# Kernel tuning notes

Hardware: AMD Instinct MI355X
Metric: run time of the kernel (lower is better)

## Reference

```python
import jax, jax.numpy as jnp
import numpy as np

CHUNK = 4096
DECAY = 0.99
EPS = 1e-5


def setup_inputs() -> dict:
    key = jax.random.key(0)
    k1, k2, k3, k4 = jax.random.split(key, 4)
    z = jax.random.normal(k1, (32, 64, 32, 32), dtype=jnp.float32)
    codebook = jax.random.normal(k2, (8192, 64), dtype=jnp.float32)
    cluster_size = jax.random.uniform(k3, (8192,), dtype=jnp.float32)
    embed_avg = jax.random.normal(k4, (8192, 64), dtype=jnp.float32)
    return {"z": z, "codebook": codebook, "cluster_size": cluster_size, "embed_avg": embed_avg}


def _nearest_indices(vectors, codebook):
    """Chunked fp32 squared-L2 nearest-neighbor search (matches _nearest_indices)."""
    cb = codebook.astype(jnp.float32)
    c2 = jnp.sum(cb * cb, axis=1)  # [K]

    def chunk_fn(chunk):
        v = chunk.astype(jnp.float32)  # [CHUNK, D]
        d = jnp.sum(v * v, axis=1, keepdims=True) + c2[None, :] - 2.0 * (v @ cb.T)
        return jnp.argmin(d, axis=1)

    n, d = vectors.shape  # n divisible by CHUNK by construction
    chunks = vectors.reshape(n // CHUNK, CHUNK, d)
    return jax.lax.map(chunk_fn, chunks).reshape(-1)


def reference(z, codebook, cluster_size, embed_avg):
    B, C, H, W = z.shape
    K = codebook.shape[0]
    # [B,C,H,W] -> [N,C]
    vectors = jnp.transpose(z, (0, 2, 3, 1)).reshape(-1, C)
    N = vectors.shape[0]

    indices = _nearest_indices(vectors, codebook)  # [N] int
    quantized = jnp.transpose(codebook[indices].reshape(B, H, W, C), (0, 3, 1, 2))

    # commitment loss (codebook learned via EMA, so only encoder side differentiable)
    vq_loss = jnp.mean((jax.lax.stop_gradient(quantized) - z) ** 2)
    # straight-through estimator
    quantized_st = z + jax.lax.stop_gradient(quantized - z)

    # code usage statistics
    counts = jax.ops.segment_sum(jnp.ones((N,), jnp.float32), indices, num_segments=K)
    avg_probs = counts / N
    perplexity = jnp.exp(-jnp.sum(avg_probs * jnp.log(avg_probs + 1e-10)))
    active_codes = jnp.sum(counts > 0).astype(jnp.int32)

    # EMA update (scatter-add accumulation + Laplace-smoothed normalization)
    sums = jax.ops.segment_sum(vectors.astype(jnp.float32), indices, num_segments=K)
    new_cluster_size = DECAY * cluster_size + (1.0 - DECAY) * counts
    new_embed_avg = DECAY * embed_avg + (1.0 - DECAY) * sums
    n_total = jnp.sum(new_cluster_size)
    smoothed = (new_cluster_size + EPS) / (n_total + K * EPS) * n_total
    new_codebook = new_embed_avg / smoothed[:, None]

    return (quantized_st, indices, vq_loss, perplexity, active_codes,
            new_codebook, new_cluster_size, new_embed_avg)
```

## Files before the change

kernel.cpp:

```cpp
#include <hip/hip_runtime.h>
#include <math.h>

typedef unsigned short u16;
typedef unsigned int u32;
typedef __attribute__((ext_vector_type(8))) short short8;
typedef __attribute__((ext_vector_type(4))) float f32x4;

#define NVEC   32768
#define DIMV   64
#define KC     8192
#define NKCH   4
#define CHK    2048
#define HW     1024
#define BPLANE 65536

#define OFF_Q    0
#define OFF_IDX  2097152
#define OFF_LOSS 2129920
#define OFF_PPL  2129921
#define OFF_ACT  2129922
#define OFF_NCB  2129923
#define OFF_NCS  2654211
#define OFF_NEA  2662403

#define WS_COUNTS 0
#define WS_SCAL   8192
#define WS_C2     8200
#define WS_CANDD  16392
#define WS_CANDI  147464
#define WS_CBH    278536
#define WS_CBM    540680
#define WS_CBL    802824

__device__ __forceinline__ u16 f2bf(float x) {
    u32 u = __float_as_uint(x);
    u += 0x7fffu + ((u >> 16) & 1u);
    return (u16)(u >> 16);
}
__device__ __forceinline__ float bf2f(u16 h) {
    return __uint_as_float(((u32)h) << 16);
}

__global__ __launch_bounds__(256) void cbsplit_kernel(const float* __restrict__ cb,
                                                      u16* __restrict__ cbh,
                                                      u16* __restrict__ cbm,
                                                      u16* __restrict__ cbl,
                                                      float* __restrict__ c2) {
    const int t = threadIdx.x;
    const int k = blockIdx.x * 4 + (t >> 6);
    const int d = t & 63;
    const int idx = k * DIMV + d;
    float x = cb[idx];
    u16 hb = f2bf(x);  float fh = bf2f(hb);
    float r1 = x - fh; u16 mb = f2bf(r1); float fm = bf2f(mb);
    float r2 = r1 - fm; u16 lb = f2bf(r2);
    cbh[idx] = hb; cbm[idx] = mb; cbl[idx] = lb;
    float s = x * x;
    for (int off = 32; off > 0; off >>= 1) s += __shfl_down(s, off, 64);
    if (d == 0) c2[k] = s;
}

__global__ __launch_bounds__(256, 2) void nn_kernel(const float* __restrict__ z,
                                                    const u16* __restrict__ cbh,
                                                    const u16* __restrict__ cbm,
                                                    const u16* __restrict__ cbl,
                                                    const float* __restrict__ c2,
                                                    float* __restrict__ candD,
                                                    int* __restrict__ candI) {
    const int l  = threadIdx.x & 63;
    const int w  = threadIdx.x >> 6;
    const int vg = blockIdx.x;
    const int kc = blockIdx.y;
    const int m0 = vg * 256 + w * 64;
    const int lr = l & 15;
    const int lg = l >> 4;

    short8 A[4][3][2];
#pragma unroll
    for (int i = 0; i < 4; ++i) {
        const int vec = m0 + i * 16 + lr;
        const float* zp = z + (size_t)(vec >> 10) * BPLANE + (vec & 1023);
#pragma unroll
        for (int s = 0; s < 2; ++s) {
            short8 ah, am, al;
#pragma unroll
            for (int e = 0; e < 8; ++e) {
                const int k = s * 32 + lg * 8 + e;
                float x = zp[k * HW];
                u16 hb = f2bf(x);   float fh = bf2f(hb);
                float r1 = x - fh;  u16 mb = f2bf(r1); float fm = bf2f(mb);
                float r2 = r1 - fm; u16 lb = f2bf(r2);
                ah[e] = (short)hb; am[e] = (short)mb; al[e] = (short)lb;
            }
            A[i][0][s] = ah; A[i][1][s] = am; A[i][2][s] = al;
        }
    }

    float bestv[4][4];
    int   bestn[4][4];
#pragma unroll
    for (int i = 0; i < 4; ++i)
#pragma unroll
        for (int r = 0; r < 4; ++r) { bestv[i][r] = -3.4e38f; bestn[i][r] = 0; }

    const int code_base = kc * CHK;
    const u16* ph = cbh + (size_t)(code_base + lr) * DIMV + lg * 8;
    const u16* pm = cbm + (size_t)(code_base + lr) * DIMV + lg * 8;
    const u16* pl = cbl + (size_t)(code_base + lr) * DIMV + lg * 8;
    const float* pc2 = c2 + code_base + lr;

    for (int nt = 0; nt < CHK / 16; ++nt) {
        const int to = nt * 16 * DIMV;
        const float cm = -0.5f * pc2[nt * 16];
        short8 Bh0 = *(const short8*)(ph + to);
        short8 Bh1 = *(const short8*)(ph + to + 32);
        short8 Bm0 = *(const short8*)(pm + to);
        short8 Bm1 = *(const short8*)(pm + to + 32);
        short8 Bl0 = *(const short8*)(pl + to);
        short8 Bl1 = *(const short8*)(pl + to + 32);
#pragma unroll
        for (int i = 0; i < 4; ++i) {
            f32x4 acc = {cm, cm, cm, cm};
            acc = __builtin_amdgcn_mfma_f32_16x16x32_bf16(A[i][0][0], Bh0, acc, 0, 0, 0);
            acc = __builtin_amdgcn_mfma_f32_16x16x32_bf16(A[i][0][1], Bh1, acc, 0, 0, 0);
            acc = __builtin_amdgcn_mfma_f32_16x16x32_bf16(A[i][1][0], Bh0, acc, 0, 0, 0);
            acc = __builtin_amdgcn_mfma_f32_16x16x32_bf16(A[i][1][1], Bh1, acc, 0, 0, 0);
            acc = __builtin_amdgcn_mfma_f32_16x16x32_bf16(A[i][0][0], Bm0, acc, 0, 0, 0);
            acc = __builtin_amdgcn_mfma_f32_16x16x32_bf16(A[i][0][1], Bm1, acc, 0, 0, 0);
            acc = __builtin_amdgcn_mfma_f32_16x16x32_bf16(A[i][1][0], Bm0, acc, 0, 0, 0);
            acc = __builtin_amdgcn_mfma_f32_16x16x32_bf16(A[i][1][1], Bm1, acc, 0, 0, 0);
            acc = __builtin_amdgcn_mfma_f32_16x16x32_bf16(A[i][2][0], Bh0, acc, 0, 0, 0);
            acc = __builtin_amdgcn_mfma_f32_16x16x32_bf16(A[i][2][1], Bh1, acc, 0, 0, 0);
            acc = __builtin_amdgcn_mfma_f32_16x16x32_bf16(A[i][0][0], Bl0, acc, 0, 0, 0);
            acc = __builtin_amdgcn_mfma_f32_16x16x32_bf16(A[i][0][1], Bl1, acc, 0, 0, 0);
#pragma unroll
            for (int r = 0; r < 4; ++r) {
                float a = acc[r];
                if (a > bestv[i][r]) { bestv[i][r] = a; bestn[i][r] = nt; }
            }
        }
    }

#pragma unroll
    for (int i = 0; i < 4; ++i)
#pragma unroll
        for (int r = 0; r < 4; ++r) {
            float v = bestv[i][r];
            int idx = bestn[i][r] * 16 + lr;
#pragma unroll
            for (int mk = 1; mk < 16; mk <<= 1) {
                float ov = __shfl_xor(v, mk, 64);
                int   oi = __shfl_xor(idx, mk, 64);
                if (ov > v || (ov == v && oi < idx)) { v = ov; idx = oi; }
            }
            if (lr == 0) {
                const int vec = m0 + i * 16 + lg * 4 + r;
                candD[kc * NVEC + vec] = -v;
                candI[kc * NVEC + vec] = code_base + idx;
            }
        }
}

__global__ __launch_bounds__(256) void gather_kernel(const float* __restrict__ z,
                                                     const float* __restrict__ cb,
                                                     const float* __restrict__ candD,
                                                     const int* __restrict__ candI,
                                                     float* __restrict__ out,
                                                     float* __restrict__ counts,
                                                     float* __restrict__ scal) {
    const int n = blockIdx.x * 256 + threadIdx.x;
    float best = 3.5e38f;
    int bi = 0;
#pragma unroll
    for (int kc = 0; kc < NKCH; ++kc) {
        float dv = candD[kc * NVEC + n];
        int iv = candI[kc * NVEC + n];
        if (dv < best) { best = dv; bi = iv; }
    }
    out[OFF_IDX + n] = (float)bi;
    atomicAdd(&counts[bi], 1.0f);

    const int b = n >> 10, h = n & 1023;
    const float* zp = z + (size_t)b * BPLANE + h;
    const float* cp = cb + (size_t)bi * DIMV;
    float* qp = out + OFF_Q + (size_t)b * BPLANE + h;
    float acc = 0.f;
#pragma unroll
    for (int c = 0; c < DIMV; ++c) {
        float zv = zp[c * HW];
        float q = cp[c];
        float df = q - zv;
        acc = fmaf(df, df, acc);
        qp[c * HW] = zv + df;
    }
    for (int off = 32; off > 0; off >>= 1) acc += __shfl_down(acc, off, 64);
    __shared__ float red[4];
    if ((threadIdx.x & 63) == 0) red[threadIdx.x >> 6] = acc;
    __syncthreads();
    if (threadIdx.x == 0) atomicAdd(&scal[0], (red[0] + red[1]) + (red[2] + red[3]));
}

__global__ __launch_bounds__(256) void prefix_kernel(const float* __restrict__ counts,
                                                     int* __restrict__ offs) {
    __shared__ int part[256];
    const int t = threadIdx.x;
    const int base = t * 32;
    int loc[32];
    int s = 0;
#pragma unroll
    for (int j = 0; j < 32; ++j) { loc[j] = s; s += (int)counts[base + j]; }
    part[t] = s;
    __syncthreads();
    for (int off = 1; off < 256; off <<= 1) {
        int v = (t >= off) ? part[t - off] : 0;
        __syncthreads();
        part[t] += v;
        __syncthreads();
    }
    const int excl = part[t] - s;
#pragma unroll
    for (int j = 0; j < 32; ++j) offs[base + j] = excl + loc[j];
}

__global__ __launch_bounds__(256) void scatter_kernel(const float* __restrict__ outIdx,
                                                      int* __restrict__ offs,
                                                      int* __restrict__ perm) {
    const int n = blockIdx.x * 256 + threadIdx.x;
    const int bi = (int)outIdx[n];
    const int pos = atomicAdd(&offs[bi], 1);
    perm[pos] = n;
}

__global__ __launch_bounds__(256) void segsum_kernel(const float* __restrict__ z,
                                                     const float* __restrict__ counts,
                                                     const int* __restrict__ offs,
                                                     const int* __restrict__ perm,
                                                     float* __restrict__ sums) {
    const int w = threadIdx.x >> 6;
    const int c = threadIdx.x & 63;
    const int k = blockIdx.x * 4 + w;
    const int end = offs[k];
    const int cnt = (int)counts[k];
    float s = 0.f;
    for (int m = end - cnt; m < end; ++m) {
        const int n = perm[m];
        s += z[(size_t)(n >> 10) * BPLANE + (size_t)c * HW + (n & 1023)];
    }
    sums[k * DIMV + c] = s;
}

__global__ __launch_bounds__(256) void emavec_kernel(const float* __restrict__ ea,
                                                     const float* __restrict__ sums,
                                                     float* __restrict__ out) {
    const int i = blockIdx.x * 256 + threadIdx.x;
    out[OFF_NEA + i] = 0.99f * ea[i] + 0.01f * sums[i];
}

__global__ __launch_bounds__(256) void stats_kernel(const float* __restrict__ cs,
                                                    const float* __restrict__ counts,
                                                    float* __restrict__ out,
                                                    float* __restrict__ scal) {
    const int k = blockIdx.x * 256 + threadIdx.x;
    const float cnt = counts[k];
    float ncs = 0.99f * cs[k] + 0.01f * cnt;
    out[OFF_NCS + k] = ncs;
    float p = cnt * (1.0f / 32768.0f);
    float pl = p * logf(p + 1e-10f);
    float act = (cnt > 0.f) ? 1.f : 0.f;
    for (int off = 32; off > 0; off >>= 1) {
        ncs += __shfl_down(ncs, off, 64);
        pl  += __shfl_down(pl,  off, 64);
        act += __shfl_down(act, off, 64);
    }
    __shared__ float r0[4], r1[4], r2[4];
    const int w = threadIdx.x >> 6;
    if ((threadIdx.x & 63) == 0) { r0[w] = ncs; r1[w] = pl; r2[w] = act; }
    __syncthreads();
    if (threadIdx.x == 0) {
        atomicAdd(&scal[1], (r0[0] + r0[1]) + (r0[2] + r0[3]));
        atomicAdd(&scal[2], (r1[0] + r1[1]) + (r1[2] + r1[3]));
        atomicAdd(&scal[3], (r2[0] + r2[1]) + (r2[2] + r2[3]));
    }
}

__global__ __launch_bounds__(256) void final_kernel(float* __restrict__ out,
                                                    const float* __restrict__ scal) {
    const int i = blockIdx.x * 256 + threadIdx.x;
    const float nt = scal[1];
    const int k = i >> 6;
    const float ncs = out[OFF_NCS + k];
    const float sm = ((ncs + 1e-5f) / (nt + 0.08192f)) * nt;
    out[OFF_NCB + i] = out[OFF_NEA + i] / sm;
    if (i == 0) {
        out[OFF_LOSS] = scal[0] * (1.0f / 2097152.0f);
        out[OFF_PPL]  = expf(-scal[2]);
        out[OFF_ACT]  = scal[3];
    }
}

extern "C" void kernel_launch(void* const* d_in, const int* in_sizes, int n_in,
                              void* d_out, int out_size, void* d_ws, size_t ws_size,
                              hipStream_t stream) {
    const float* z  = (const float*)d_in[0];
    const float* cb = (const float*)d_in[1];
    const float* cs = (const float*)d_in[2];
    const float* ea = (const float*)d_in[3];
    float* out = (float*)d_out;
    float* ws  = (float*)d_ws;

    float* counts = ws + WS_COUNTS;
    float* scal   = ws + WS_SCAL;
    float* c2     = ws + WS_C2;
    float* candD  = ws + WS_CANDD;
    int*   candI  = (int*)(ws + WS_CANDI);
    u16*   cbh    = (u16*)(ws + WS_CBH);
    u16*   cbm    = (u16*)(ws + WS_CBM);
    u16*   cbl    = (u16*)(ws + WS_CBL);
    int*   perm   = (int*)(ws + WS_CANDD);
    int*   offs   = (int*)(ws + WS_CANDI);
    float* sums   = ws + WS_CBH;

    hipMemsetAsync(ws, 0, (8192 + 8) * 4, stream);
    cbsplit_kernel<<<KC / 4, 256, 0, stream>>>(cb, cbh, cbm, cbl, c2);
    nn_kernel<<<dim3(128, 4), 256, 0, stream>>>(z, cbh, cbm, cbl, c2, candD, candI);
    gather_kernel<<<NVEC / 256, 256, 0, stream>>>(z, cb, candD, candI, out, counts, scal);
    prefix_kernel<<<1, 256, 0, stream>>>(counts, offs);
    scatter_kernel<<<NVEC / 256, 256, 0, stream>>>(out + OFF_IDX, offs, perm);
    segsum_kernel<<<KC / 4, 256, 0, stream>>>(z, counts, offs, perm, sums);
    emavec_kernel<<<524288 / 256, 256, 0, stream>>>(ea, sums, out);
    stats_kernel<<<KC / 256, 256, 0, stream>>>(cs, counts, out, scal);
    final_kernel<<<524288 / 256, 256, 0, stream>>>(out, scal);
}
```

Measured before the change: 296.9 us.

## Split NN search finer, merge candidates via packed 64-bit atomicMin, fuse EMA kernel

The codebook is split into 8 chunks instead of 4, and each block now covers 128 vectors instead of 256, so the grid grows from 512 to 2048 blocks and the launch bound allows higher occupancy. Per-chunk candidates are merged with a 64-bit atomicMin on a packed (monotone distance, index) key instead of writing candidate arrays and reducing them in the gather kernel. The separate EMA-vector kernel is folded into the final kernel. This trades a larger grid, less A-register reuse per B load and atomic contention for more parallelism and fewer passes over memory.

```diff
diff --git a/kernel.cpp b/kernel.cpp
--- a/kernel.cpp
+++ b/kernel.cpp
@@ -3,14 +3,15 @@
 
 typedef unsigned short u16;
 typedef unsigned int u32;
+typedef unsigned long long u64;
 typedef __attribute__((ext_vector_type(8))) short short8;
 typedef __attribute__((ext_vector_type(4))) float f32x4;
 
 #define NVEC   32768
 #define DIMV   64
 #define KC     8192
-#define NKCH   4
-#define CHK    2048
+#define NKCH   8
+#define CHK    1024
 #define HW     1024
 #define BPLANE 65536
 
@@ -26,11 +27,12 @@
 #define WS_COUNTS 0
 #define WS_SCAL   8192
 #define WS_C2     8200
-#define WS_CANDD  16392
-#define WS_CANDI  147464
-#define WS_CBH    278536
-#define WS_CBM    540680
-#define WS_CBL    802824
+#define WS_MINP   16400
+#define WS_OFFS   81936
+#define WS_PERM   90128
+#define WS_CBH    122896
+#define WS_CBM    385040
+#define WS_CBL    647184
 
 __device__ __forceinline__ u16 f2bf(float x) {
     u32 u = __float_as_uint(x);
@@ -39,6 +41,10 @@
 }
 __device__ __forceinline__ float bf2f(u16 h) {
     return __uint_as_float(((u32)h) << 16);
+}
+__device__ __forceinline__ u32 fmono(float f) {
+    u32 b = __float_as_uint(f);
+    return (b & 0x80000000u) ? ~b : (b | 0x80000000u);
 }
 
 __global__ __launch_bounds__(256) void cbsplit_kernel(const float* __restrict__ cb,
@@ -60,24 +66,23 @@
     if (d == 0) c2[k] = s;
 }
 
-__global__ __launch_bounds__(256, 2) void nn_kernel(const float* __restrict__ z,
+__global__ __launch_bounds__(256, 4) void nn_kernel(const float* __restrict__ z,
                                                     const u16* __restrict__ cbh,
                                                     const u16* __restrict__ cbm,
                                                     const u16* __restrict__ cbl,
                                                     const float* __restrict__ c2,
-                                                    float* __restrict__ candD,
-                                                    int* __restrict__ candI) {
+                                                    u64* __restrict__ minp) {
     const int l  = threadIdx.x & 63;
     const int w  = threadIdx.x >> 6;
     const int vg = blockIdx.x;
     const int kc = blockIdx.y;
-    const int m0 = vg * 256 + w * 64;
+    const int m0 = vg * 128 + w * 32;
     const int lr = l & 15;
     const int lg = l >> 4;
 
-    short8 A[4][3][2];
-#pragma unroll
-    for (int i = 0; i < 4; ++i) {
+    short8 A[2][3][2];
+#pragma unroll
+    for (int i = 0; i < 2; ++i) {
         const int vec = m0 + i * 16 + lr;
         const float* zp = z + (size_t)(vec >> 10) * BPLANE + (vec & 1023);
 #pragma unroll
@@ -96,10 +101,10 @@
         }
     }
 
-    float bestv[4][4];
-    int   bestn[4][4];
-#pragma unroll
-    for (int i = 0; i < 4; ++i)
+    float bestv[2][4];
+    int   bestn[2][4];
+#pragma unroll
+    for (int i = 0; i < 2; ++i)
 #pragma unroll
         for (int r = 0; r < 4; ++r) { bestv[i][r] = -3.4e38f; bestn[i][r] = 0; }
 
@@ -119,7 +124,7 @@
         short8 Bl0 = *(const short8*)(pl + to);
         short8 Bl1 = *(const short8*)(pl + to + 32);
 #pragma unroll
-        for (int i = 0; i < 4; ++i) {
+        for (int i = 0; i < 2; ++i) {
             f32x4 acc = {cm, cm, cm, cm};
             acc = __builtin_amdgcn_mfma_f32_16x16x32_bf16(A[i][0][0], Bh0, acc, 0, 0, 0);
             acc = __builtin_amdgcn_mfma_f32_16x16x32_bf16(A[i][0][1], Bh1, acc, 0, 0, 0);
@@ -142,7 +147,7 @@
     }
 
 #pragma unroll
-    for (int i = 0; i < 4; ++i)
+    for (int i = 0; i < 2; ++i)
 #pragma unroll
         for (int r = 0; r < 4; ++r) {
             float v = bestv[i][r];
@@ -155,28 +160,20 @@
             }
             if (lr == 0) {
                 const int vec = m0 + i * 16 + lg * 4 + r;
-                candD[kc * NVEC + vec] = -v;
-                candI[kc * NVEC + vec] = code_base + idx;
+                const u64 pack = ((u64)fmono(-v) << 32) | (u32)(code_base + idx);
+                atomicMin(&minp[vec], pack);
             }
         }
 }
 
 __global__ __launch_bounds__(256) void gather_kernel(const float* __restrict__ z,
                                                      const float* __restrict__ cb,
-                                                     const float* __restrict__ candD,
-                                                     const int* __restrict__ candI,
+                                                     const u64* __restrict__ minp,
                                                      float* __restrict__ out,
                                                      float* __restrict__ counts,
                                                      float* __restrict__ scal) {
     const int n = blockIdx.x * 256 + threadIdx.x;
-    float best = 3.5e38f;
-    int bi = 0;
-#pragma unroll
-    for (int kc = 0; kc < NKCH; ++kc) {
-        float dv = candD[kc * NVEC + n];
-        int iv = candI[kc * NVEC + n];
-        if (dv < best) { best = dv; bi = iv; }
-    }
+    const int bi = (int)(u32)(minp[n] & 0xFFFFFFFFu);
     out[OFF_IDX + n] = (float)bi;
     atomicAdd(&counts[bi], 1.0f);
 
@@ -247,13 +244,6 @@
         s += z[(size_t)(n >> 10) * BPLANE + (size_t)c * HW + (n & 1023)];
     }
     sums[k * DIMV + c] = s;
-}
-
-__global__ __launch_bounds__(256) void emavec_kernel(const float* __restrict__ ea,
-                                                     const float* __restrict__ sums,
-                                                     float* __restrict__ out) {
-    const int i = blockIdx.x * 256 + threadIdx.x;
-    out[OFF_NEA + i] = 0.99f * ea[i] + 0.01f * sums[i];
 }
 
 __global__ __launch_bounds__(256) void stats_kernel(const float* __restrict__ cs,
@@ -283,14 +273,18 @@
     }
 }
 
-__global__ __launch_bounds__(256) void final_kernel(float* __restrict__ out,
+__global__ __launch_bounds__(256) void final_kernel(const float* __restrict__ ea,
+                                                    const float* __restrict__ sums,
+                                                    float* __restrict__ out,
                                                     const float* __restrict__ scal) {
     const int i = blockIdx.x * 256 + threadIdx.x;
+    const float nea = 0.99f * ea[i] + 0.01f * sums[i];
+    out[OFF_NEA + i] = nea;
     const float nt = scal[1];
     const int k = i >> 6;
     const float ncs = out[OFF_NCS + k];
     const float sm = ((ncs + 1e-5f) / (nt + 0.08192f)) * nt;
-    out[OFF_NCB + i] = out[OFF_NEA + i] / sm;
+    out[OFF_NCB + i] = nea / sm;
     if (i == 0) {
         out[OFF_LOSS] = scal[0] * (1.0f / 2097152.0f);
         out[OFF_PPL]  = expf(-scal[2]);
@@ -311,23 +305,22 @@
     float* counts = ws + WS_COUNTS;
     float* scal   = ws + WS_SCAL;
     float* c2     = ws + WS_C2;
-    float* candD  = ws + WS_CANDD;
-    int*   candI  = (int*)(ws + WS_CANDI);
+    u64*   minp   = (u64*)(ws + WS_MINP);
+    int*   offs   = (int*)(ws + WS_OFFS);
+    int*   perm   = (int*)(ws + WS_PERM);
     u16*   cbh    = (u16*)(ws + WS_CBH);
     u16*   cbm    = (u16*)(ws + WS_CBM);
     u16*   cbl    = (u16*)(ws + WS_CBL);
-    int*   perm   = (int*)(ws + WS_CANDD);
-    int*   offs   = (int*)(ws + WS_CANDI);
     float* sums   = ws + WS_CBH;
 
-    hipMemsetAsync(ws, 0, (8192 + 8) * 4, stream);
+    hipMemsetAsync(ws, 0, 8200 * 4, stream);
+    hipMemsetAsync(minp, 0xFF, NVEC * 8, stream);
     cbsplit_kernel<<<KC / 4, 256, 0, stream>>>(cb, cbh, cbm, cbl, c2);
-    nn_kernel<<<dim3(128, 4), 256, 0, stream>>>(z, cbh, cbm, cbl, c2, candD, candI);
-    gather_kernel<<<NVEC / 256, 256, 0, stream>>>(z, cb, candD, candI, out, counts, scal);
+    nn_kernel<<<dim3(256, NKCH), 256, 0, stream>>>(z, cbh, cbm, cbl, c2, minp);
+    gather_kernel<<<NVEC / 256, 256, 0, stream>>>(z, cb, minp, out, counts, scal);
     prefix_kernel<<<1, 256, 0, stream>>>(counts, offs);
     scatter_kernel<<<NVEC / 256, 256, 0, stream>>>(out + OFF_IDX, offs, perm);
     segsum_kernel<<<KC / 4, 256, 0, stream>>>(z, counts, offs, perm, sums);
-    emavec_kernel<<<524288 / 256, 256, 0, stream>>>(ea, sums, out);
     stats_kernel<<<KC / 256, 256, 0, stream>>>(cs, counts, out, scal);
-    final_kernel<<<524288 / 256, 256, 0, stream>>>(out, scal);
-}
+    final_kernel<<<524288 / 256, 256, 0, stream>>>(ea, sums, out, scal);
+}
```

Measured after the change: 460.9 us. 1.55x slower.
